# Kernel tuning notes

Hardware: AMD Instinct MI355X
Metric: run time of the kernel (lower is better)

## Reference

```python
import jax, jax.numpy as jnp
import numpy as np

D_MODEL = 1024
NUM_HEADS = 16
D_K = 1024
D_V = 1024
D_IN = 1024
THETA = 10000.0
B, S = 2, 2048


def setup_inputs() -> dict:
    key = jax.random.key(0)
    k1, k2, k3, k4, k5 = jax.random.split(key, 5)
    std_qkv = (2.0 / (D_IN + D_K)) ** 0.5
    std_o = (2.0 / (D_V + D_MODEL)) ** 0.5
    x = jax.random.normal(k1, (B, S, D_IN), jnp.float32)
    wq = jax.random.normal(k2, (D_IN, D_K), jnp.float32) * std_qkv
    wk = jax.random.normal(k3, (D_IN, D_K), jnp.float32) * std_qkv
    wv = jax.random.normal(k4, (D_IN, D_V), jnp.float32) * std_qkv
    wo = jax.random.normal(k5, (D_V, D_MODEL), jnp.float32) * std_o
    return {"x": x, "wq": wq, "wk": wk, "wv": wv, "wo": wo}


def _rope(t, theta):
    # t: (H, B, S, hd) -- interleaved-pair RoPE, angles pos * theta^(-2i/hd)
    hd = t.shape[-1]
    inv_freq = 1.0 / (theta ** (jnp.arange(0, hd, 2, dtype=jnp.float32) / hd))  # (hd/2,)
    pos = jnp.arange(t.shape[-2], dtype=jnp.float32)
    ang = pos[:, None] * inv_freq[None, :]                                       # (S, hd/2)
    cos, sin = jnp.cos(ang), jnp.sin(ang)
    tp = t.reshape(t.shape[:-1] + (hd // 2, 2))
    t0, t1 = tp[..., 0], tp[..., 1]
    out = jnp.stack([t0 * cos - t1 * sin, t0 * sin + t1 * cos], axis=-1)
    return out.reshape(t.shape)


def reference(x, wq, wk, wv, wo):
    b, s, _ = x.shape
    hd = D_K // NUM_HEADS
    hdv = D_V // NUM_HEADS
    # fused QKV proj (math identical to concat-then-matmul)
    q = jnp.einsum('bsd,de->bse', x, wq).reshape(b, s, NUM_HEADS, hd).transpose(2, 0, 1, 3)
    k = jnp.einsum('bsd,de->bse', x, wk).reshape(b, s, NUM_HEADS, hd).transpose(2, 0, 1, 3)
    v = jnp.einsum('bsd,de->bse', x, wv).reshape(b, s, NUM_HEADS, hdv).transpose(2, 0, 1, 3)
    q = _rope(q, THETA)
    k = _rope(k, THETA)
    scale = 1.0 / jnp.sqrt(jnp.asarray(hd, jnp.float32))
    scores = jnp.einsum('hbqd,hbkd->hbqk', q, k) * scale                 # (H,B,S,S)
    causal = jnp.tril(jnp.ones((s, s), dtype=bool))
    scores = jnp.where(causal, scores, -jnp.inf)
    attn = jax.nn.softmax(scores, axis=-1)
    o = jnp.einsum('hbqk,hbkd->hbqd', attn, v)                            # (H,B,S,hdv)
    o = o.transpose(1, 2, 0, 3).reshape(b, s, D_V)                        # merge heads (outer)
    return jnp.einsum('bsd,de->bse', o, wo)
```

## Files before the change

### kernel.cpp

```cpp
#include <hip/hip_runtime.h>
#include <stdint.h>

typedef __attribute__((ext_vector_type(8))) short short8;
typedef __attribute__((ext_vector_type(4))) float f32x4;
typedef __attribute__((ext_vector_type(16))) float f32x16;
typedef __attribute__((ext_vector_type(4))) unsigned short ushort4v;
typedef __attribute__((ext_vector_type(2))) unsigned int uint2v;

static __device__ __forceinline__ unsigned short f2b(float f) {
  union { float f; unsigned int u; } v; v.f = f;
  unsigned int r = v.u + 0x7FFFu + ((v.u >> 16) & 1u);
  return (unsigned short)(r >> 16);
}

static __device__ __forceinline__ float exp2fast(float x) {
#if __has_builtin(__builtin_amdgcn_exp2f)
  return __builtin_amdgcn_exp2f(x);
#else
  return exp2f(x);
#endif
}

static __device__ __forceinline__ unsigned int cvtpk(float lo, float hi) {
  unsigned int r;
  asm("v_cvt_pk_bf16_f32 %0, %1, %2" : "=v"(r) : "v"(lo), "v"(hi));
  return r;
}

static __device__ __forceinline__ float xor32max(float x) {
#if __has_builtin(__builtin_amdgcn_permlane32_swap)
  unsigned u = __float_as_uint(x);
  uint2v r = __builtin_amdgcn_permlane32_swap(u, u, false, false);
  return fmaxf(__uint_as_float(r[0]), __uint_as_float(r[1]));
#else
  return fmaxf(x, __shfl_xor(x, 32));
#endif
}
static __device__ __forceinline__ float xor32add(float x) {
#if __has_builtin(__builtin_amdgcn_permlane32_swap)
  unsigned u = __float_as_uint(x);
  uint2v r = __builtin_amdgcn_permlane32_swap(u, u, false, false);
  return __uint_as_float(r[0]) + __uint_as_float(r[1]);
#else
  return x + __shfl_xor(x, 32);
#endif
}

static __device__ __forceinline__ void gload16(const void* g, void* l) {
  __builtin_amdgcn_global_load_lds(
      (const __attribute__((address_space(1))) unsigned int*)g,
      (__attribute__((address_space(3))) unsigned int*)l, 16, 0, 0);
}


__global__ __launch_bounds__(256) void cast_x_kernel(const float* __restrict__ x,
                                                     unsigned short* __restrict__ xb) {
  int i = (blockIdx.x * 256 + threadIdx.x) * 4;
  float4 v = *(const float4*)(x + i);
  ushort4v o = { f2b(v.x), f2b(v.y), f2b(v.z), f2b(v.w) };
  *(ushort4v*)(xb + i) = o;
}

__global__ __launch_bounds__(256) void transpose_cast_kernel(
    const float* __restrict__ wq, const float* __restrict__ wk,
    const float* __restrict__ wv, const float* __restrict__ wo,
    unsigned short* __restrict__ wT) {
  const int z = blockIdx.z;
  const float* src = (z == 0) ? wq : (z == 1) ? wk : (z == 2) ? wv : wo;
  unsigned short* dst = wT + (size_t)z * 1048576;
  __shared__ float t[32][33];
  const int tid = threadIdx.x;
  const int tx = tid & 31, ty = tid >> 5;
  const int n0 = blockIdx.x * 32, k0 = blockIdx.y * 32;
#pragma unroll
  for (int i = 0; i < 4; ++i) {
    int r = ty + i * 8;
    t[r][tx] = src[(size_t)(k0 + r) * 1024 + n0 + tx];
  }
  __syncthreads();
#pragma unroll
  for (int i = 0; i < 4; ++i) {
    int r = ty + i * 8;
    dst[(size_t)(n0 + r) * 1024 + k0 + tx] = f2b(t[tx][r]);
  }
}

__global__ __launch_bounds__(256) void rope_tab_kernel(float* __restrict__ ct,
                                                       float* __restrict__ st) {
  int i = blockIdx.x * 256 + threadIdx.x;
  int s = i >> 5, p = i & 31;
  float ang = (float)s * powf(10000.0f, -(float)(2 * p) / 64.0f);
  ct[i] = cosf(ang);
  st[i] = sinf(ang);
}


__global__ __launch_bounds__(256) void gemm_kernel(
    const unsigned short* __restrict__ A, const unsigned short* __restrict__ WT,
    unsigned short* __restrict__ Qb, unsigned short* __restrict__ Kb,
    unsigned short* __restrict__ VTb, float* __restrict__ Fout,
    const float* __restrict__ ctab, const float* __restrict__ stab, int finalMode) {
  __shared__ unsigned short As[128 * 32];
  __shared__ unsigned short Bs[128 * 32];
  const int tid = threadIdx.x;
  const int w = tid >> 6, lane = tid & 63;
  const int m0 = blockIdx.x * 128, n0 = blockIdx.y * 128;
  int mode;
  const unsigned short* Bt;
  if (finalMode) { mode = 3; Bt = WT; }
  else { mode = blockIdx.z; Bt = WT + (size_t)mode * 1048576; }
  const int wr = w >> 1, wc = w & 1;
  const int srow = lane >> 2, scol = lane & 3;
  f32x4 acc[4][4] = {};
  for (int k0 = 0; k0 < 1024; k0 += 32) {
#pragma unroll
    for (int c = 0; c < 2; ++c) {
      int chunk = w * 2 + c;
      gload16(A + (size_t)(m0 + chunk * 16 + srow) * 1024 + k0 + scol * 8,
              (char*)As + chunk * 1024);
      gload16(Bt + (size_t)(n0 + chunk * 16 + srow) * 1024 + k0 + scol * 8,
              (char*)Bs + chunk * 1024);
    }
    __syncthreads();
    short8 af[4], bf[4];
#pragma unroll
    for (int i = 0; i < 4; ++i) {
      af[i] = *(const short8*)((const char*)As +
              ((wr * 64 + i * 16 + (lane & 15)) * 64 + (lane >> 4) * 16));
      bf[i] = *(const short8*)((const char*)Bs +
              ((wc * 64 + i * 16 + (lane & 15)) * 64 + (lane >> 4) * 16));
    }
#pragma unroll
    for (int i = 0; i < 4; ++i)
#pragma unroll
      for (int j = 0; j < 4; ++j)
        acc[i][j] = __builtin_amdgcn_mfma_f32_16x16x32_bf16(af[i], bf[j], acc[i][j], 0, 0, 0);
    __syncthreads();
  }

  if (mode < 2) {
    unsigned short* dst = mode ? Kb : Qb;
    const float qscale = mode ? 1.0f : 0.125f * 1.44269504088896f;
#pragma unroll
    for (int i = 0; i < 4; ++i) {
#pragma unroll
      for (int j = 0; j < 4; ++j) {
        int n = n0 + wc * 64 + j * 16 + (lane & 15);
        int h = n >> 6, d = n & 63;
        int pairIdx = d >> 1;
        bool even = (n & 1) == 0;
#pragma unroll
        for (int r = 0; r < 4; ++r) {
          int m = m0 + wr * 64 + i * 16 + (lane >> 4) * 4 + r;
          int b = m >> 11, s = m & 2047;
          float v = acc[i][j][r];
          float pv = __shfl_xor(v, 1);
          float c = ctab[s * 32 + pairIdx], sn = stab[s * 32 + pairIdx];
          float ov = (even ? (v * c - pv * sn) : (pv * sn + v * c)) * qscale;
          dst[(size_t)((h * 2 + b) * 2048 + s) * 64 + d] = f2b(ov);
        }
      }
    }
  } else if (mode == 2) {
#pragma unroll
    for (int i = 0; i < 4; ++i) {
#pragma unroll
      for (int j = 0; j < 4; ++j) {
        int n = n0 + wc * 64 + j * 16 + (lane & 15);
        int h = n >> 6, d = n & 63;
        int mBase = m0 + wr * 64 + i * 16 + (lane >> 4) * 4;
        int b = mBase >> 11, s = mBase & 2047;
        ushort4v pk = { f2b(acc[i][j][0]), f2b(acc[i][j][1]),
                        f2b(acc[i][j][2]), f2b(acc[i][j][3]) };
        *(ushort4v*)(VTb + (size_t)((h * 2 + b) * 64 + d) * 2048 + s) = pk;
      }
    }
  } else {
#pragma unroll
    for (int i = 0; i < 4; ++i)
#pragma unroll
      for (int j = 0; j < 4; ++j) {
        int n = n0 + wc * 64 + j * 16 + (lane & 15);
#pragma unroll
        for (int r = 0; r < 4; ++r) {
          int m = m0 + wr * 64 + i * 16 + (lane >> 4) * 4 + r;
          Fout[(size_t)m * 1024 + n] = acc[i][j][r];
        }
      }
  }
}


__global__ __launch_bounds__(256) void attn_kernel(
    const unsigned short* __restrict__ Qb, const unsigned short* __restrict__ Kb,
    const unsigned short* __restrict__ VTb, unsigned short* __restrict__ Ob) {
  __shared__ unsigned short Ks[2][64 * 64];
  __shared__ unsigned short Vs[2][64 * 64];
  const int tid = threadIdx.x, w = tid >> 6, lane = tid & 63;
  const int lq = lane & 31, hi = lane >> 5;
  const int hb = blockIdx.y;
  const int bxx = blockIdx.x ^ ((hb >> 4) << 3);
  const int qt = (bxx < 8) ? bxx : 23 - bxx;
  const int h = hb >> 1, b = hb & 1;
  const unsigned short* Qhb = Qb + (size_t)hb * 2048 * 64;
  const unsigned short* Khb = Kb + (size_t)hb * 2048 * 64;
  const unsigned short* Vhb = VTb + (size_t)hb * 64 * 2048;
  const int qbase = qt * 128 + w * 32;
  const int swq = (lq & 7) << 4;
  const int ktmax = 2 * qt + 1;

  short8 qf[4];
#pragma unroll
  for (int s = 0; s < 4; ++s)
    qf[s] = *(const short8*)(Qhb + (size_t)(qbase + lq) * 64 + s * 16 + hi * 8);

  const f32x16 Z16 = {0,0,0,0,0,0,0,0,0,0,0,0,0,0,0,0};
  f32x16 o0 = Z16, o1 = Z16;
  float m = -__builtin_inff(), ls = 0.f;

  const int r0 = tid >> 3, f0 = tid & 7;
  const int so0 = r0 * 128 + ((f0 * 16) ^ ((r0 & 7) << 4));
  short8 gK[2], gV[2];
  gK[0] = *(const short8*)(Khb + (size_t)r0 * 64 + f0 * 8);
  gK[1] = *(const short8*)(Khb + (size_t)(r0 + 32) * 64 + f0 * 8);
  gV[0] = *(const short8*)(Vhb + (size_t)r0 * 2048 + f0 * 8);
  gV[1] = *(const short8*)(Vhb + (size_t)(r0 + 32) * 2048 + f0 * 8);
  *(short8*)((char*)Ks[0] + so0) = gK[0];
  *(short8*)((char*)Ks[0] + so0 + 32 * 128) = gK[1];
  *(short8*)((char*)Vs[0] + so0) = gV[0];
  *(short8*)((char*)Vs[0] + so0 + 32 * 128) = gV[1];
  __syncthreads();

  for (int kt = 0; kt <= ktmax; ++kt) {
    const int cur = kt & 1;
    if (kt < ktmax) {
      int kk0 = (kt + 1) * 64;
      gK[0] = *(const short8*)(Khb + (size_t)(kk0 + r0) * 64 + f0 * 8);
      gK[1] = *(const short8*)(Khb + (size_t)(kk0 + r0 + 32) * 64 + f0 * 8);
      gV[0] = *(const short8*)(Vhb + (size_t)r0 * 2048 + kk0 + f0 * 8);
      gV[1] = *(const short8*)(Vhb + (size_t)(r0 + 32) * 2048 + kk0 + f0 * 8);
    }
    if (kt * 64 <= qbase + 31) {
      const unsigned short* Ksb = Ks[cur];
      const unsigned short* Vsb = Vs[cur];
      f32x16 s0 = Z16, s1 = Z16;
      __builtin_amdgcn_s_setprio(1);
#pragma unroll
      for (int st = 0; st < 4; ++st) {
        short8 a0 = *(const short8*)((const char*)Ksb + lq * 128 +
                    ((st * 32 + hi * 16) ^ swq));
        short8 a1 = *(const short8*)((const char*)Ksb + (32 + lq) * 128 +
                    ((st * 32 + hi * 16) ^ swq));
        s0 = __builtin_amdgcn_mfma_f32_32x32x16_bf16(a0, qf[st], s0, 0, 0, 0);
        s1 = __builtin_amdgcn_mfma_f32_32x32x16_bf16(a1, qf[st], s1, 0, 0, 0);
      }
      __builtin_amdgcn_s_setprio(0);

      if (kt * 64 + 63 > qbase) {
        int relk = qbase + lq - kt * 64;
#pragma unroll
        for (int r = 0; r < 16; ++r) {
          int km = (r & 3) + 8 * (r >> 2) + 4 * hi;
          if (km > relk) s0[r] = -__builtin_inff();
          if (km + 32 > relk) s1[r] = -__builtin_inff();
        }
      }

      float mx = s0[0];
#pragma unroll
      for (int r = 1; r < 16; ++r) mx = fmaxf(mx, s0[r]);
#pragma unroll
      for (int r = 0; r < 16; ++r) mx = fmaxf(mx, s1[r]);
      mx = xor32max(mx);
      float nm = fmaxf(m, mx);
      float al = exp2fast(m - nm);
      m = nm;
      float ps = 0.f;
#pragma unroll
      for (int r = 0; r < 16; ++r) { float p = exp2fast(s0[r] - nm); s0[r] = p; ps += p; }
#pragma unroll
      for (int r = 0; r < 16; ++r) { float p = exp2fast(s1[r] - nm); s1[r] = p; ps += p; }
      ls = ls * al + ps;
      o0 *= al;
      o1 *= al;

      unsigned int pk0[8], pk1[8];
#pragma unroll
      for (int jp = 0; jp < 8; ++jp) {
        pk0[jp] = cvtpk(s0[2 * jp], s0[2 * jp + 1]);
        pk1[jp] = cvtpk(s1[2 * jp], s1[2 * jp + 1]);
      }
      __builtin_amdgcn_s_setprio(1);
#pragma unroll
      for (int ks = 0; ks < 4; ++ks) {
        const int off = 4 * (ks & 1);
        unsigned int a0 = (ks < 2) ? pk0[off + 0] : pk1[off + 0];
        unsigned int a1 = (ks < 2) ? pk0[off + 1] : pk1[off + 1];
        unsigned int b0 = (ks < 2) ? pk0[off + 2] : pk1[off + 2];
        unsigned int b1 = (ks < 2) ? pk0[off + 3] : pk1[off + 3];
        uint2v w0 = __builtin_amdgcn_permlane32_swap(a0, b0, false, false);
        uint2v w1 = __builtin_amdgcn_permlane32_swap(a1, b1, false, false);
        union { unsigned int u[4]; short8 s; } F;
        F.u[0] = w0[0]; F.u[1] = w1[0]; F.u[2] = w0[1]; F.u[3] = w1[1];
        short8 v0 = *(const short8*)((const char*)Vsb + lq * 128 +
                    ((ks * 32 + hi * 16) ^ swq));
        short8 v1 = *(const short8*)((const char*)Vsb + (32 + lq) * 128 +
                    ((ks * 32 + hi * 16) ^ swq));
        o0 = __builtin_amdgcn_mfma_f32_32x32x16_bf16(v0, F.s, o0, 0, 0, 0);
        o1 = __builtin_amdgcn_mfma_f32_32x32x16_bf16(v1, F.s, o1, 0, 0, 0);
      }
      __builtin_amdgcn_s_setprio(0);
    }
    if (kt < ktmax) {
      *(short8*)((char*)Ks[cur ^ 1] + so0) = gK[0];
      *(short8*)((char*)Ks[cur ^ 1] + so0 + 32 * 128) = gK[1];
      *(short8*)((char*)Vs[cur ^ 1] + so0) = gV[0];
      *(short8*)((char*)Vs[cur ^ 1] + so0 + 32 * 128) = gV[1];
    }
    __syncthreads();
  }

  ls = xor32add(ls);
  float invl = 1.0f / ls;
  char* Osw = (char*)Ks + w * 4096;
#pragma unroll
  for (int jp = 0; jp < 8; ++jp) {
    const int r = 2 * jp;
    const int km = (r & 3) + 8 * (r >> 2) + 4 * hi;
    unsigned int pa = cvtpk(o0[r] * invl, o0[r + 1] * invl);
    unsigned int pb = cvtpk(o1[r] * invl, o1[r + 1] * invl);
    *(unsigned int*)(Osw + lq * 128 + ((2 * km) ^ swq)) = pa;
    *(unsigned int*)(Osw + lq * 128 + ((2 * (km + 32)) ^ swq)) = pb;
  }
  __builtin_amdgcn_wave_barrier();
#pragma unroll
  for (int pass = 0; pass < 4; ++pass) {
    int q2 = pass * 8 + (lane >> 3);
    int c16 = (lane & 7) * 16;
    short8 vrow = *(const short8*)(Osw + q2 * 128 + (c16 ^ ((q2 & 7) << 4)));
    int srow = qbase + q2;
    *(short8*)(Ob + (size_t)(b * 2048 + srow) * 1024 + h * 64 + (lane & 7) * 8) = vrow;
  }
}


extern "C" void kernel_launch(void* const* d_in, const int* in_sizes, int n_in,
                              void* d_out, int out_size, void* d_ws, size_t ws_size,
                              hipStream_t stream) {
  const float* x  = (const float*)d_in[0];
  const float* wq = (const float*)d_in[1];
  const float* wk = (const float*)d_in[2];
  const float* wv = (const float*)d_in[3];
  const float* wo = (const float*)d_in[4];
  float* out = (float*)d_out;

  char* ws = (char*)d_ws;
  const size_t SZ = 8388608;
  unsigned short* xb  = (unsigned short*)(ws);
  unsigned short* wT  = (unsigned short*)(ws + SZ);
  unsigned short* Qb  = (unsigned short*)(ws + 2 * SZ);
  unsigned short* Kb  = (unsigned short*)(ws + 3 * SZ);
  unsigned short* VTb = (unsigned short*)(ws + 4 * SZ);
  unsigned short* Ob  = (unsigned short*)(ws + 5 * SZ);
  float* ctab = (float*)(ws + 6 * SZ);
  float* stab = (float*)(ws + 6 * SZ + 262144);
  if (ws_size < 6 * SZ + 2 * 262144) return;

  cast_x_kernel<<<4096, 256, 0, stream>>>(x, xb);
  transpose_cast_kernel<<<dim3(32, 32, 4), 256, 0, stream>>>(wq, wk, wv, wo, wT);
  rope_tab_kernel<<<256, 256, 0, stream>>>(ctab, stab);
  gemm_kernel<<<dim3(32, 8, 3), 256, 0, stream>>>(xb, wT, Qb, Kb, VTb, nullptr, ctab, stab, 0);
  attn_kernel<<<dim3(16, 32), 256, 0, stream>>>(Qb, Kb, VTb, Ob);
  gemm_kernel<<<dim3(32, 8, 1), 256, 0, stream>>>(Ob, wT + 3 * 1048576, Qb, Kb, VTb, out,
                                                  ctab, stab, 1);
}
```

Measured before the change: 138.9 us.

## Fuse prep kernels, add dedicated output GEMM, use lazy softmax rescaling

Merges the x cast, weight transpose-cast and RoPE table kernels into one launch to cut launch overhead. The output projection moves to its own GEMM kernel with 64x128 tiles and 128 threads, doubling the block count from 256 to 512 so more CUs are busy. In attention, the online softmax now rescales the running max and accumulators only when some lane's new max exceeds the old one by more than 8 (in log2 units), and the row-sum is accumulated with split partial sums. The lazy rescale can let exponentials grow up to 2^8 before renormalising, which is still safe in fp32 but changes rounding slightly.

Result: faster. 135.4 us (-2.5%).

```diff
diff --git a/kernel.cpp b/kernel.cpp
--- a/kernel.cpp
+++ b/kernel.cpp
@@ -53,62 +53,59 @@
 }
 
 
-__global__ __launch_bounds__(256) void cast_x_kernel(const float* __restrict__ x,
-                                                     unsigned short* __restrict__ xb) {
-  int i = (blockIdx.x * 256 + threadIdx.x) * 4;
-  float4 v = *(const float4*)(x + i);
-  ushort4v o = { f2b(v.x), f2b(v.y), f2b(v.z), f2b(v.w) };
-  *(ushort4v*)(xb + i) = o;
-}
-
-__global__ __launch_bounds__(256) void transpose_cast_kernel(
-    const float* __restrict__ wq, const float* __restrict__ wk,
-    const float* __restrict__ wv, const float* __restrict__ wo,
-    unsigned short* __restrict__ wT) {
-  const int z = blockIdx.z;
-  const float* src = (z == 0) ? wq : (z == 1) ? wk : (z == 2) ? wv : wo;
-  unsigned short* dst = wT + (size_t)z * 1048576;
+__global__ __launch_bounds__(256) void prep_kernel(
+    const float* __restrict__ x, const float* __restrict__ wq,
+    const float* __restrict__ wk, const float* __restrict__ wv,
+    const float* __restrict__ wo, unsigned short* __restrict__ xb,
+    unsigned short* __restrict__ wT, float* __restrict__ ct,
+    float* __restrict__ st) {
   __shared__ float t[32][33];
-  const int tid = threadIdx.x;
-  const int tx = tid & 31, ty = tid >> 5;
-  const int n0 = blockIdx.x * 32, k0 = blockIdx.y * 32;
-#pragma unroll
-  for (int i = 0; i < 4; ++i) {
-    int r = ty + i * 8;
-    t[r][tx] = src[(size_t)(k0 + r) * 1024 + n0 + tx];
-  }
-  __syncthreads();
-#pragma unroll
-  for (int i = 0; i < 4; ++i) {
-    int r = ty + i * 8;
-    dst[(size_t)(n0 + r) * 1024 + k0 + tx] = f2b(t[tx][r]);
-  }
-}
-
-__global__ __launch_bounds__(256) void rope_tab_kernel(float* __restrict__ ct,
-                                                       float* __restrict__ st) {
-  int i = blockIdx.x * 256 + threadIdx.x;
-  int s = i >> 5, p = i & 31;
-  float ang = (float)s * powf(10000.0f, -(float)(2 * p) / 64.0f);
-  ct[i] = cosf(ang);
-  st[i] = sinf(ang);
+  const int bid = blockIdx.x, tid = threadIdx.x;
+  if (bid < 4096) {
+    int i = (bid * 256 + tid) * 4;
+    float4 v = *(const float4*)(x + i);
+    ushort4v o = { f2b(v.x), f2b(v.y), f2b(v.z), f2b(v.w) };
+    *(ushort4v*)(xb + i) = o;
+  } else if (bid < 8192) {
+    int tt = bid - 4096;
+    int z = tt >> 10, xy = tt & 1023;
+    const float* src = (z == 0) ? wq : (z == 1) ? wk : (z == 2) ? wv : wo;
+    unsigned short* dst = wT + (size_t)z * 1048576;
+    int tx = tid & 31, ty = tid >> 5;
+    int n0 = (xy & 31) * 32, k0 = (xy >> 5) * 32;
+#pragma unroll
+    for (int i = 0; i < 4; ++i) {
+      int r = ty + i * 8;
+      t[r][tx] = src[(size_t)(k0 + r) * 1024 + n0 + tx];
+    }
+    __syncthreads();
+#pragma unroll
+    for (int i = 0; i < 4; ++i) {
+      int r = ty + i * 8;
+      dst[(size_t)(n0 + r) * 1024 + k0 + tx] = f2b(t[tx][r]);
+    }
+  } else {
+    int i = (bid - 8192) * 256 + tid;
+    int s = i >> 5, p = i & 31;
+    float ang = (float)s * powf(10000.0f, -(float)(2 * p) / 64.0f);
+    ct[i] = cosf(ang);
+    st[i] = sinf(ang);
+  }
 }
 
 
 __global__ __launch_bounds__(256) void gemm_kernel(
     const unsigned short* __restrict__ A, const unsigned short* __restrict__ WT,
     unsigned short* __restrict__ Qb, unsigned short* __restrict__ Kb,
-    unsigned short* __restrict__ VTb, float* __restrict__ Fout,
-    const float* __restrict__ ctab, const float* __restrict__ stab, int finalMode) {
+    unsigned short* __restrict__ VTb,
+    const float* __restrict__ ctab, const float* __restrict__ stab) {
   __shared__ unsigned short As[128 * 32];
   __shared__ unsigned short Bs[128 * 32];
   const int tid = threadIdx.x;
   const int w = tid >> 6, lane = tid & 63;
   const int m0 = blockIdx.x * 128, n0 = blockIdx.y * 128;
-  int mode;
-  const unsigned short* Bt;
-  if (finalMode) { mode = 3; Bt = WT; }
-  else { mode = blockIdx.z; Bt = WT + (size_t)mode * 1048576; }
+  const int mode = blockIdx.z;
+  const unsigned short* Bt = WT + (size_t)mode * 1048576;
   const int wr = w >> 1, wc = w & 1;
   const int srow = lane >> 2, scol = lane & 3;
   f32x4 acc[4][4] = {};
@@ -161,7 +158,7 @@
         }
       }
     }
-  } else if (mode == 2) {
+  } else {
 #pragma unroll
     for (int i = 0; i < 4; ++i) {
 #pragma unroll
@@ -175,19 +172,60 @@
         *(ushort4v*)(VTb + (size_t)((h * 2 + b) * 64 + d) * 2048 + s) = pk;
       }
     }
-  } else {
+  }
+}
+
+
+__global__ __launch_bounds__(128) void gemm_final_kernel(
+    const unsigned short* __restrict__ A, const unsigned short* __restrict__ Bt,
+    float* __restrict__ Fout) {
+  __shared__ unsigned short As[64 * 32];
+  __shared__ unsigned short Bs[128 * 32];
+  const int tid = threadIdx.x;
+  const int w = tid >> 6, lane = tid & 63;
+  const int m0 = blockIdx.x * 64, n0 = blockIdx.y * 128;
+  const int srow = lane >> 2, scol = lane & 3;
+  f32x4 acc[4][4] = {};
+  for (int k0 = 0; k0 < 1024; k0 += 32) {
+#pragma unroll
+    for (int c = 0; c < 2; ++c) {
+      int chunk = w * 2 + c;
+      gload16(A + (size_t)(m0 + chunk * 16 + srow) * 1024 + k0 + scol * 8,
+              (char*)As + chunk * 1024);
+    }
+#pragma unroll
+    for (int c = 0; c < 4; ++c) {
+      int chunk = w * 4 + c;
+      gload16(Bt + (size_t)(n0 + chunk * 16 + srow) * 1024 + k0 + scol * 8,
+              (char*)Bs + chunk * 1024);
+    }
+    __syncthreads();
+    short8 af[4], bf[4];
+#pragma unroll
+    for (int i = 0; i < 4; ++i) {
+      af[i] = *(const short8*)((const char*)As +
+              ((i * 16 + (lane & 15)) * 64 + (lane >> 4) * 16));
+      bf[i] = *(const short8*)((const char*)Bs +
+              ((w * 64 + i * 16 + (lane & 15)) * 64 + (lane >> 4) * 16));
+    }
 #pragma unroll
     for (int i = 0; i < 4; ++i)
 #pragma unroll
-      for (int j = 0; j < 4; ++j) {
-        int n = n0 + wc * 64 + j * 16 + (lane & 15);
-#pragma unroll
-        for (int r = 0; r < 4; ++r) {
-          int m = m0 + wr * 64 + i * 16 + (lane >> 4) * 4 + r;
-          Fout[(size_t)m * 1024 + n] = acc[i][j][r];
-        }
-      }
-  }
+      for (int j = 0; j < 4; ++j)
+        acc[i][j] = __builtin_amdgcn_mfma_f32_16x16x32_bf16(af[i], bf[j], acc[i][j], 0, 0, 0);
+    __syncthreads();
+  }
+#pragma unroll
+  for (int i = 0; i < 4; ++i)
+#pragma unroll
+    for (int j = 0; j < 4; ++j) {
+      int n = n0 + w * 64 + j * 16 + (lane & 15);
+#pragma unroll
+      for (int r = 0; r < 4; ++r) {
+        int m = m0 + i * 16 + (lane >> 4) * 4 + r;
+        Fout[(size_t)m * 1024 + n] = acc[i][j][r];
+      }
+    }
 }
 
 
@@ -266,23 +304,37 @@
         }
       }
 
-      float mx = s0[0];
-#pragma unroll
-      for (int r = 1; r < 16; ++r) mx = fmaxf(mx, s0[r]);
-#pragma unroll
-      for (int r = 0; r < 16; ++r) mx = fmaxf(mx, s1[r]);
-      mx = xor32max(mx);
-      float nm = fmaxf(m, mx);
-      float al = exp2fast(m - nm);
-      m = nm;
-      float ps = 0.f;
-#pragma unroll
-      for (int r = 0; r < 16; ++r) { float p = exp2fast(s0[r] - nm); s0[r] = p; ps += p; }
-#pragma unroll
-      for (int r = 0; r < 16; ++r) { float p = exp2fast(s1[r] - nm); s1[r] = p; ps += p; }
-      ls = ls * al + ps;
-      o0 *= al;
-      o1 *= al;
+      float t8[8];
+#pragma unroll
+      for (int r = 0; r < 8; ++r)
+        t8[r] = fmaxf(fmaxf(s0[2 * r], s0[2 * r + 1]),
+                      fmaxf(s1[2 * r], s1[2 * r + 1]));
+      float mA = fmaxf(fmaxf(t8[0], t8[1]), fmaxf(t8[2], t8[3]));
+      float mB = fmaxf(fmaxf(t8[4], t8[5]), fmaxf(t8[6], t8[7]));
+      float mx = xor32max(fmaxf(mA, mB));
+
+      if (__any(mx > m + 8.0f)) {
+        float nm = fmaxf(m, mx);
+        float al = exp2fast(m - nm);
+        m = nm;
+        ls *= al;
+        o0 *= al;
+        o1 *= al;
+      }
+      float ps0 = 0.f, ps1 = 0.f, ps2 = 0.f, ps3 = 0.f;
+#pragma unroll
+      for (int r = 0; r < 16; ++r) {
+        float p = exp2fast(s0[r] - m);
+        s0[r] = p;
+        if (r < 8) ps0 += p; else ps1 += p;
+      }
+#pragma unroll
+      for (int r = 0; r < 16; ++r) {
+        float p = exp2fast(s1[r] - m);
+        s1[r] = p;
+        if (r < 8) ps2 += p; else ps3 += p;
+      }
+      ls += (ps0 + ps1) + (ps2 + ps3);
 
       unsigned int pk0[8], pk1[8];
 #pragma unroll
@@ -366,11 +418,8 @@
   float* stab = (float*)(ws + 6 * SZ + 262144);
   if (ws_size < 6 * SZ + 2 * 262144) return;
 
-  cast_x_kernel<<<4096, 256, 0, stream>>>(x, xb);
-  transpose_cast_kernel<<<dim3(32, 32, 4), 256, 0, stream>>>(wq, wk, wv, wo, wT);
-  rope_tab_kernel<<<256, 256, 0, stream>>>(ctab, stab);
-  gemm_kernel<<<dim3(32, 8, 3), 256, 0, stream>>>(xb, wT, Qb, Kb, VTb, nullptr, ctab, stab, 0);
+  prep_kernel<<<8448, 256, 0, stream>>>(x, wq, wk, wv, wo, xb, wT, ctab, stab);
+  gemm_kernel<<<dim3(32, 8, 3), 256, 0, stream>>>(xb, wT, Qb, Kb, VTb, ctab, stab);
   attn_kernel<<<dim3(16, 32), 256, 0, stream>>>(Qb, Kb, VTb, Ob);
-  gemm_kernel<<<dim3(32, 8, 1), 256, 0, stream>>>(Ob, wT + 3 * 1048576, Qb, Kb, VTb, out,
-                                                  ctab, stab, 1);
-}
+  gemm_final_kernel<<<dim3(64, 8), 128, 0, stream>>>(Ob, wT + 3 * 1048576, out);
+}
```
